# Kernel tuning notes

Measured on AMD Instinct MI355X. Metric: run time of the kernel, lower is better.

The kernel has to match this reference:

```python
import jax, jax.numpy as jnp
import numpy as np

N_NODES = 100000
N_EDGES = 3200000
F_IN = 1433
HID = 16
N_CLS = 7


def setup_inputs() -> dict:
    key = jax.random.key(0)
    k1, k2, k3, k4 = jax.random.split(key, 4)
    x = jax.random.normal(k1, (N_NODES, F_IN), dtype=jnp.float32)
    edge_index = jax.random.randint(k2, (2, N_EDGES), 0, N_NODES, dtype=jnp.int32)
    # Glorot-style init like GCNConv
    W1 = jax.random.normal(k3, (F_IN, HID), dtype=jnp.float32) * (1.0 / np.sqrt(F_IN))
    b1 = jnp.zeros((HID,), dtype=jnp.float32)
    W2 = jax.random.normal(k4, (HID, N_CLS), dtype=jnp.float32) * (1.0 / np.sqrt(HID))
    b2 = jnp.zeros((N_CLS,), dtype=jnp.float32)
    return {"x": x, "edge_index": edge_index, "W1": W1, "b1": b1, "W2": W2, "b2": b2}


def _gcn_conv(h, src, dst, W, b):
    # GCNConv with normalize=False: dense transform, then unweighted sum-aggregate
    # over incoming edges plus a self-loop (add_self_loops=True default), then bias.
    t = h @ W                                   # [N, out]
    agg = jax.ops.segment_sum(t[src], dst, num_segments=N_NODES)  # scatter-add over edges
    return agg + t + b                          # '+ t' = self-loop contribution


def reference(x, edge_index, W1, b1, W2, b2):
    src, dst = edge_index[0], edge_index[1]
    h = jax.nn.relu(_gcn_conv(x, src, dst, W1, b1))
    # F.dropout(training=False) is identity in eval mode
    out = _gcn_conv(h, src, dst, W2, b2)
    return out
```

## Files before the change

kernel.cpp:

```cpp
#include <hip/hip_runtime.h>

#define N_NODES 100000
#define N_EDGES 3200000
#define F_IN    1433
#define HID     16
#define N_CLS   7
#define NWINT   48
#define GB1     (N_NODES / 16)
#define QBLK    (N_EDGES / 4 / 256)
#define NTOT    ((long)N_NODES * F_IN)
#define NBKT    1024
#define NPBK    98
#define BCAP2   512
#define SRCM    0x1FFFF

typedef __attribute__((ext_vector_type(8))) short short8v;
typedef __attribute__((ext_vector_type(4))) float float4v;

typedef const __attribute__((address_space(1))) unsigned* gptr_t;
typedef __attribute__((address_space(3))) unsigned* lptr_t;

__device__ __forceinline__ unsigned short f2bf(float f) {
    unsigned u = __float_as_uint(f);
    u += 0x7fffu + ((u >> 16) & 1u);
    return (unsigned short)(u >> 16);
}

__device__ __forceinline__ void gll16(const float* g, float* lds) {
    gptr_t gp = (gptr_t)(unsigned long long)(uintptr_t)g;
    lptr_t lp = (lptr_t)(unsigned)(uintptr_t)lds;
    __builtin_amdgcn_global_load_lds(gp, lp, 16, 0, 0);
}

__global__ void prep_w1_kernel(const float* __restrict__ W1, short* __restrict__ w1f) {
    int w = blockIdx.x;
    int l = threadIdx.x;
    int col = l & 15;
    int kb = w * 32 + (l >> 4) * 8;
    short8v f;
#pragma unroll
    for (int i = 0; i < 8; ++i) {
        int k = kb + i;
        float v = (k < F_IN) ? W1[k * HID + col] : 0.f;
        f[i] = (short)f2bf(v);
    }
    *(short8v*)(w1f + ((size_t)w * 64 + l) * 8) = f;
}

__device__ __noinline__ void gemm_arm(int gid, const float* __restrict__ x,
                                      const short* __restrict__ w1f,
                                      float* __restrict__ t1) {
    __shared__ float xs[3][16][128];
    const int tid = threadIdx.x;
    const int s = tid >> 6;
    const int l = tid & 63;
    const int R0 = gid * 16;
    const int g = l >> 4;
    const int c = l & 15;

    short8v bf[12];
#pragma unroll
    for (int ph = 0; ph < 12; ++ph)
        bf[ph] = *(const short8v*)(w1f + ((size_t)((ph * 4 + s) * 64 + l)) * 8);

    const int row_a = 2 * s + (l >> 5);
    const int cs = l & 31;
    const bool last = (gid == GB1 - 1);

#define ISSUE(ph_)                                                              \
    {                                                                           \
        _Pragma("unroll")                                                       \
        for (int i = 0; i < 2; ++i) {                                           \
            int row = i * 8 + row_a;                                            \
            int gch = cs ^ (row & 7);                                           \
            long gi = (long)(R0 + row) * F_IN + (ph_) * 128 + gch * 4;          \
            if (last && gi > NTOT - 4) gi = NTOT - 4;                           \
            gll16(x + gi, &xs[(ph_) % 3][i * 8 + 2 * s][0]);                    \
        }                                                                       \
    }

    ISSUE(0); ISSUE(1);

    const int p0 = ((s * 8 + 2 * g) ^ (c & 7)) * 4;
    const int p1 = ((s * 8 + 2 * g + 1) ^ (c & 7)) * 4;

    float4v acc = {0.f, 0.f, 0.f, 0.f};
#pragma unroll
    for (int ph = 0; ph < 12; ++ph) {
        if (ph < 11) asm volatile("s_waitcnt vmcnt(2)" ::: "memory");
        else         asm volatile("s_waitcnt vmcnt(0)" ::: "memory");
        __builtin_amdgcn_sched_barrier(0);
        __builtin_amdgcn_s_barrier();
        if (ph + 2 < 12) ISSUE(ph + 2);
        const float* rowp = &xs[ph % 3][c][0];
        float4 lo = *(const float4*)(rowp + p0);
        float4 hi = *(const float4*)(rowp + p1);
        short8v af;
        af[0] = (short)f2bf(lo.x); af[1] = (short)f2bf(lo.y);
        af[2] = (short)f2bf(lo.z); af[3] = (short)f2bf(lo.w);
        af[4] = (short)f2bf(hi.x); af[5] = (short)f2bf(hi.y);
        af[6] = (short)f2bf(hi.z); af[7] = (short)f2bf(hi.w);
        acc = __builtin_amdgcn_mfma_f32_16x16x32_bf16(af, bf[ph], acc, 0, 0, 0);
    }
#undef ISSUE

    float* reds = &xs[0][0][0] + s * 256;
#pragma unroll
    for (int j = 0; j < 4; ++j) reds[l * 4 + j] = acc[j];
    __syncthreads();
    {
        int r = tid >> 4, cc = tid & 15;
        int idx = ((r >> 2) * 16 + cc) * 4 + (r & 3);
        float* rb = &xs[0][0][0];
        float vv = rb[idx] + rb[256 + idx] + rb[512 + idx] + rb[768 + idx];
        t1[(long)(R0 + r) * HID + cc] = vv;
    }
}

__device__ __noinline__ void fill_arm(int fbid, const int* __restrict__ src,
                                      const int* __restrict__ dst,
                                      int* __restrict__ cnt, int* __restrict__ bkt) {
    const int p = blockIdx.x & 7;
    int i = fbid * 256 + threadIdx.x;
    int4 s4 = ((const int4*)src)[i];
    int4 d4 = ((const int4*)dst)[i];
    unsigned b, dl; int pos;
    b = (unsigned)d4.x / NPBK; dl = (unsigned)d4.x - b * NPBK;
    pos = atomicAdd(&cnt[(p << 10) + b], 1);
    if (pos < BCAP2) bkt[((size_t)((p << 10) + b) << 9) + pos] = (int)((dl << 17) | (unsigned)s4.x);
    b = (unsigned)d4.y / NPBK; dl = (unsigned)d4.y - b * NPBK;
    pos = atomicAdd(&cnt[(p << 10) + b], 1);
    if (pos < BCAP2) bkt[((size_t)((p << 10) + b) << 9) + pos] = (int)((dl << 17) | (unsigned)s4.y);
    b = (unsigned)d4.z / NPBK; dl = (unsigned)d4.z - b * NPBK;
    pos = atomicAdd(&cnt[(p << 10) + b], 1);
    if (pos < BCAP2) bkt[((size_t)((p << 10) + b) << 9) + pos] = (int)((dl << 17) | (unsigned)s4.z);
    b = (unsigned)d4.w / NPBK; dl = (unsigned)d4.w - b * NPBK;
    pos = atomicAdd(&cnt[(p << 10) + b], 1);
    if (pos < BCAP2) bkt[((size_t)((p << 10) + b) << 9) + pos] = (int)((dl << 17) | (unsigned)s4.w);
}

__global__ __launch_bounds__(256) void fat1_kernel(const float* __restrict__ x,
                                                   const short* __restrict__ w1f,
                                                   float* __restrict__ t1,
                                                   const int* __restrict__ src,
                                                   const int* __restrict__ dst,
                                                   int* __restrict__ cnt,
                                                   int* __restrict__ bkt) {
    const int bid = blockIdx.x;
    if (bid % 3 == 2) fill_arm((bid - 2) / 3, src, dst, cnt, bkt);
    else              gemm_arm(bid - (bid + 1) / 3, x, w1f, t1);
}

__global__ __launch_bounds__(256) void agg1f_kernel(const float* __restrict__ t1,
                                                    const int* __restrict__ cnt,
                                                    const int* __restrict__ bkt,
                                                    const float* __restrict__ b1,
                                                    const float* __restrict__ W2,
                                                    float* __restrict__ t2p) {
    __shared__ int els[4096];
    __shared__ int ecsr[4096];
    __shared__ int dcnt[128], doff[128], dcur[128];
    __shared__ int pbase[9];
    __shared__ float hl[NPBK][16];
    const int b = blockIdx.x;
    const int t = threadIdx.x;
    if (t == 0) {
        int s = 0;
        for (int p = 0; p < 8; ++p) {
            pbase[p] = s;
            int ne = cnt[(p << 10) + b]; if (ne > BCAP2) ne = BCAP2;
            s += ne;
        }
        pbase[8] = s;
    }
    if (t < 128) dcnt[t] = 0;
    __syncthreads();
    const int nt = pbase[8];
    for (int p = 0; p < 8; ++p) {
        int base0 = pbase[p], ne = pbase[p + 1] - base0;
        const int* __restrict__ bp = bkt + ((size_t)((p << 10) + b) << 9);
        for (int e = t; e < ne; e += 256) els[base0 + e] = bp[e];
    }
    __syncthreads();
    for (int e = t; e < nt; e += 256) atomicAdd(&dcnt[els[e] >> 17], 1);
    __syncthreads();
    if (t < 128) doff[t] = dcnt[t];
    __syncthreads();
    for (int d = 1; d < 128; d <<= 1) {
        int add = (t < 128 && t >= d) ? doff[t - d] : 0;
        __syncthreads();
        if (t < 128) doff[t] += add;
        __syncthreads();
    }
    if (t < 128) dcur[t] = doff[t] - dcnt[t];
    __syncthreads();
    for (int e = t; e < nt; e += 256) {
        int v = els[e];
        int pos = atomicAdd(&dcur[v >> 17], 1);
        ecsr[pos] = v & SRCM;
    }
    __syncthreads();
    const int nbase = b * NPBK;
    {
        int q = t & 3;
        for (int nl = t >> 2; nl < NPBK; nl += 64) {
            int node = nbase + nl;
            if (node < N_NODES) {
                int o = doff[nl] - dcnt[nl];
                int d = dcnt[nl];
                float4 a0 = *(const float4*)(t1 + ((size_t)node * 16 + q * 4));
                float4 bb = *(const float4*)(b1 + q * 4);
                a0.x += bb.x; a0.y += bb.y; a0.z += bb.z; a0.w += bb.w;
                float4 a1 = {0.f, 0.f, 0.f, 0.f};
                int e = 0;
                for (; e + 4 <= d; e += 4) {
                    int s0 = ecsr[o + e],     s1 = ecsr[o + e + 1];
                    int s2 = ecsr[o + e + 2], s3 = ecsr[o + e + 3];
                    float4 v0 = *(const float4*)(t1 + ((size_t)s0 * 16 + q * 4));
                    float4 v1 = *(const float4*)(t1 + ((size_t)s1 * 16 + q * 4));
                    float4 v2 = *(const float4*)(t1 + ((size_t)s2 * 16 + q * 4));
                    float4 v3 = *(const float4*)(t1 + ((size_t)s3 * 16 + q * 4));
                    a0.x += v0.x; a0.y += v0.y; a0.z += v0.z; a0.w += v0.w;
                    a1.x += v1.x; a1.y += v1.y; a1.z += v1.z; a1.w += v1.w;
                    a0.x += v2.x; a0.y += v2.y; a0.z += v2.z; a0.w += v2.w;
                    a1.x += v3.x; a1.y += v3.y; a1.z += v3.z; a1.w += v3.w;
                }
                for (; e < d; ++e) {
                    int s = ecsr[o + e];
                    float4 v = *(const float4*)(t1 + ((size_t)s * 16 + q * 4));
                    a0.x += v.x; a0.y += v.y; a0.z += v.z; a0.w += v.w;
                }
                float4 r = {fmaxf(a0.x + a1.x, 0.f), fmaxf(a0.y + a1.y, 0.f),
                            fmaxf(a0.z + a1.z, 0.f), fmaxf(a0.w + a1.w, 0.f)};
                *(float4*)(&hl[nl][q * 4]) = r;
            }
        }
    }
    __syncthreads();
    for (int idx = t; idx < NPBK * 8; idx += 256) {
        int ln = idx >> 3, c = idx & 7;
        int node = nbase + ln;
        if (node < N_NODES) {
            float a = 0.f;
            if (c < N_CLS) {
#pragma unroll
                for (int j = 0; j < HID; ++j) a = fmaf(hl[ln][j], W2[j * N_CLS + c], a);
            }
            t2p[(size_t)node * 8 + c] = a;
        }
    }
}

__global__ __launch_bounds__(256) void agg2_kernel(const float* __restrict__ t2p,
                                                   const int* __restrict__ cnt,
                                                   const int* __restrict__ bkt,
                                                   const float* __restrict__ b2,
                                                   float* __restrict__ out) {
    __shared__ int els[4096];
    __shared__ int ecsr[4096];
    __shared__ int dcnt[128], doff[128], dcur[128];
    __shared__ int pbase[9];
    const int b = blockIdx.x;
    const int t = threadIdx.x;
    if (t == 0) {
        int s = 0;
        for (int p = 0; p < 8; ++p) {
            pbase[p] = s;
            int ne = cnt[(p << 10) + b]; if (ne > BCAP2) ne = BCAP2;
            s += ne;
        }
        pbase[8] = s;
    }
    if (t < 128) dcnt[t] = 0;
    __syncthreads();
    const int nt = pbase[8];
    for (int p = 0; p < 8; ++p) {
        int base0 = pbase[p], ne = pbase[p + 1] - base0;
        const int* __restrict__ bp = bkt + ((size_t)((p << 10) + b) << 9);
        for (int e = t; e < ne; e += 256) els[base0 + e] = bp[e];
    }
    __syncthreads();
    for (int e = t; e < nt; e += 256) atomicAdd(&dcnt[els[e] >> 17], 1);
    __syncthreads();
    if (t < 128) doff[t] = dcnt[t];
    __syncthreads();
    for (int d = 1; d < 128; d <<= 1) {
        int add = (t < 128 && t >= d) ? doff[t - d] : 0;
        __syncthreads();
        if (t < 128) doff[t] += add;
        __syncthreads();
    }
    if (t < 128) dcur[t] = doff[t] - dcnt[t];
    __syncthreads();
    for (int e = t; e < nt; e += 256) {
        int v = els[e];
        int pos = atomicAdd(&dcur[v >> 17], 1);
        ecsr[pos] = v & SRCM;
    }
    __syncthreads();
    const int nbase = b * NPBK;
    {
        int q = t & 1;
        for (int nl = t >> 1; nl < NPBK; nl += 128) {
            int node = nbase + nl;
            if (node < N_NODES) {
                int o = doff[nl] - dcnt[nl];
                int d = dcnt[nl];
                float4 a0 = *(const float4*)(t2p + ((size_t)node * 8 + q * 4));
                if (q == 0) {
                    a0.x += b2[0]; a0.y += b2[1]; a0.z += b2[2]; a0.w += b2[3];
                } else {
                    a0.x += b2[4]; a0.y += b2[5]; a0.z += b2[6];
                }
                float4 a1 = {0.f, 0.f, 0.f, 0.f};
                int e = 0;
                for (; e + 4 <= d; e += 4) {
                    int s0 = ecsr[o + e],     s1 = ecsr[o + e + 1];
                    int s2 = ecsr[o + e + 2], s3 = ecsr[o + e + 3];
                    float4 v0 = *(const float4*)(t2p + ((size_t)s0 * 8 + q * 4));
                    float4 v1 = *(const float4*)(t2p + ((size_t)s1 * 8 + q * 4));
                    float4 v2 = *(const float4*)(t2p + ((size_t)s2 * 8 + q * 4));
                    float4 v3 = *(const float4*)(t2p + ((size_t)s3 * 8 + q * 4));
                    a0.x += v0.x; a0.y += v0.y; a0.z += v0.z; a0.w += v0.w;
                    a1.x += v1.x; a1.y += v1.y; a1.z += v1.z; a1.w += v1.w;
                    a0.x += v2.x; a0.y += v2.y; a0.z += v2.z; a0.w += v2.w;
                    a1.x += v3.x; a1.y += v3.y; a1.z += v3.z; a1.w += v3.w;
                }
                for (; e < d; ++e) {
                    int s = ecsr[o + e];
                    float4 v = *(const float4*)(t2p + ((size_t)s * 8 + q * 4));
                    a0.x += v.x; a0.y += v.y; a0.z += v.z; a0.w += v.w;
                }
                float* op = out + (size_t)node * 7 + q * 4;
                op[0] = a0.x + a1.x; op[1] = a0.y + a1.y; op[2] = a0.z + a1.z;
                if (q == 0) op[3] = a0.w + a1.w;
            }
        }
    }
}


extern "C" void kernel_launch(void* const* d_in, const int* in_sizes, int n_in,
                              void* d_out, int out_size, void* d_ws, size_t ws_size,
                              hipStream_t stream) {
    const float* x  = (const float*)d_in[0];
    const int*   ei = (const int*)d_in[1];
    const float* W1 = (const float*)d_in[2];
    const float* b1 = (const float*)d_in[3];
    const float* W2 = (const float*)d_in[4];
    const float* b2 = (const float*)d_in[5];
    const int* src = ei;
    const int* dst = ei + N_EDGES;
    float* out = (float*)d_out;

    char* w = (char*)d_ws;
    float* t1  = (float*)w;  w += (size_t)N_NODES * HID * sizeof(float);
    float* t2p = (float*)w;  w += (size_t)N_NODES * 8 * sizeof(float);
    short* w1f = (short*)w;  w += (size_t)NWINT * 64 * 8 * sizeof(short);
    int* cnt   = (int*)w;    w += (size_t)8 * NBKT * sizeof(int);
    int* bkt   = (int*)w;    w += (size_t)8 * NBKT * BCAP2 * sizeof(int);

    (void)hipMemsetAsync(cnt, 0, (size_t)8 * NBKT * sizeof(int), stream);
    prep_w1_kernel<<<NWINT, 64, 0, stream>>>(W1, w1f);

    fat1_kernel<<<GB1 + QBLK, 256, 0, stream>>>(x, w1f, t1, src, dst, cnt, bkt);

    agg1f_kernel<<<NBKT, 256, 0, stream>>>(t1, cnt, bkt, b1, W2, t2p);
    agg2_kernel<<<NBKT, 256, 0, stream>>>(t2p, cnt, bkt, b2, out);
}
```

Before: 281.8 us.

## Load whole 8-row x tiles contiguously into LDS for GEMM arm

The GEMM arm now processes 8 rows per block and loads each row's full 1433-float span contiguously into a padded LDS buffer in one burst, instead of streaming 16-row by 128-column phases through a triple buffer. Each wave covers a contiguous K range of 384, and half of the MFMA lanes feed zeros because only 8 rows are valid. The fill/gemm block interleave changes from 1:2 to 1:4 to match the doubled GEMM block count. This aims at more contiguous global reads and less per-phase barrier overhead, but it wastes half the MFMA work, uses about 48KB of LDS per block (which lowers occupancy), and gives up the load/compute overlap.

```diff
diff --git a/kernel.cpp b/kernel.cpp
--- a/kernel.cpp
+++ b/kernel.cpp
@@ -6,9 +6,10 @@
 #define HID     16
 #define N_CLS   7
 #define NWINT   48
-#define GB1     (N_NODES / 16)
+#define GB1     (N_NODES / 8)
 #define QBLK    (N_EDGES / 4 / 256)
 #define NTOT    ((long)N_NODES * F_IN)
+#define LSTR    1444
 #define NBKT    1024
 #define NPBK    98
 #define BCAP2   512
@@ -50,69 +51,69 @@
 __device__ __noinline__ void gemm_arm(int gid, const float* __restrict__ x,
                                       const short* __restrict__ w1f,
                                       float* __restrict__ t1) {
-    __shared__ float xs[3][16][128];
+    __shared__ float xs[12288];
     const int tid = threadIdx.x;
     const int s = tid >> 6;
     const int l = tid & 63;
-    const int R0 = gid * 16;
+    const int R0 = gid * 8;
     const int g = l >> 4;
     const int c = l & 15;
 
     short8v bf[12];
 #pragma unroll
-    for (int ph = 0; ph < 12; ++ph)
-        bf[ph] = *(const short8v*)(w1f + ((size_t)((ph * 4 + s) * 64 + l)) * 8);
-
-    const int row_a = 2 * s + (l >> 5);
-    const int cs = l & 31;
-    const bool last = (gid == GB1 - 1);
-
-#define ISSUE(ph_)                                                              \
-    {                                                                           \
-        _Pragma("unroll")                                                       \
-        for (int i = 0; i < 2; ++i) {                                           \
-            int row = i * 8 + row_a;                                            \
-            int gch = cs ^ (row & 7);                                           \
-            long gi = (long)(R0 + row) * F_IN + (ph_) * 128 + gch * 4;          \
-            if (last && gi > NTOT - 4) gi = NTOT - 4;                           \
-            gll16(x + gi, &xs[(ph_) % 3][i * 8 + 2 * s][0]);                    \
-        }                                                                       \
-    }
-
-    ISSUE(0); ISSUE(1);
-
-    const int p0 = ((s * 8 + 2 * g) ^ (c & 7)) * 4;
-    const int p1 = ((s * 8 + 2 * g + 1) ^ (c & 7)) * 4;
-
+    for (int wl = 0; wl < 12; ++wl)
+        bf[wl] = *(const short8v*)(w1f + ((size_t)((s * 12 + wl) * 64 + l)) * 8);
+
+    if (gid != GB1 - 1) {
+#pragma unroll
+        for (int j = 0; j < 12; ++j) {
+            int df = j * 1024 + tid * 4;
+            unsigned row = (unsigned)df / (unsigned)LSTR;
+            unsigned col = (unsigned)df - row * (unsigned)LSTR;
+            long src = (row < 8 && col < 1433)
+                           ? (long)(R0 + (int)row) * F_IN + col
+                           : 0;
+            gll16(x + src, &xs[df]);
+        }
+        __syncthreads();
+    } else {
+        for (int idx = tid; idx < 8 * LSTR; idx += 256) {
+            int row = idx / LSTR, col = idx - row * LSTR;
+            float v = (col < F_IN) ? x[(long)(R0 + row) * F_IN + col] : 0.f;
+            xs[idx] = v;
+        }
+        for (int idx = 8 * LSTR + tid; idx < 12288; idx += 256) xs[idx] = 0.f;
+        __syncthreads();
+    }
+
+    const int kb = s * 384;
+    const bool act = (c < 8);
     float4v acc = {0.f, 0.f, 0.f, 0.f};
 #pragma unroll
-    for (int ph = 0; ph < 12; ++ph) {
-        if (ph < 11) asm volatile("s_waitcnt vmcnt(2)" ::: "memory");
-        else         asm volatile("s_waitcnt vmcnt(0)" ::: "memory");
-        __builtin_amdgcn_sched_barrier(0);
-        __builtin_amdgcn_s_barrier();
-        if (ph + 2 < 12) ISSUE(ph + 2);
-        const float* rowp = &xs[ph % 3][c][0];
-        float4 lo = *(const float4*)(rowp + p0);
-        float4 hi = *(const float4*)(rowp + p1);
+    for (int wl = 0; wl < 12; ++wl) {
+        int off = c * LSTR + kb + wl * 32 + g * 8;
+        float4 lo = {0.f, 0.f, 0.f, 0.f}, hi = {0.f, 0.f, 0.f, 0.f};
+        if (act) {
+            lo = *(const float4*)(&xs[off]);
+            hi = *(const float4*)(&xs[off + 4]);
+        }
         short8v af;
         af[0] = (short)f2bf(lo.x); af[1] = (short)f2bf(lo.y);
         af[2] = (short)f2bf(lo.z); af[3] = (short)f2bf(lo.w);
         af[4] = (short)f2bf(hi.x); af[5] = (short)f2bf(hi.y);
         af[6] = (short)f2bf(hi.z); af[7] = (short)f2bf(hi.w);
-        acc = __builtin_amdgcn_mfma_f32_16x16x32_bf16(af, bf[ph], acc, 0, 0, 0);
-    }
-#undef ISSUE
-
-    float* reds = &xs[0][0][0] + s * 256;
+        acc = __builtin_amdgcn_mfma_f32_16x16x32_bf16(af, bf[wl], acc, 0, 0, 0);
+    }
+
+    __syncthreads();
+    float* reds = &xs[s * 256];
 #pragma unroll
     for (int j = 0; j < 4; ++j) reds[l * 4 + j] = acc[j];
     __syncthreads();
-    {
+    if (tid < 128) {
         int r = tid >> 4, cc = tid & 15;
         int idx = ((r >> 2) * 16 + cc) * 4 + (r & 3);
-        float* rb = &xs[0][0][0];
-        float vv = rb[idx] + rb[256 + idx] + rb[512 + idx] + rb[768 + idx];
+        float vv = xs[idx] + xs[256 + idx] + xs[512 + idx] + xs[768 + idx];
         t1[(long)(R0 + r) * HID + cc] = vv;
     }
 }
@@ -147,8 +148,8 @@
                                                    int* __restrict__ cnt,
                                                    int* __restrict__ bkt) {
     const int bid = blockIdx.x;
-    if (bid % 3 == 2) fill_arm((bid - 2) / 3, src, dst, cnt, bkt);
-    else              gemm_arm(bid - (bid + 1) / 3, x, w1f, t1);
+    if (bid % 5 == 4) fill_arm((bid - 4) / 5, src, dst, cnt, bkt);
+    else              gemm_arm(bid - (bid + 1) / 5, x, w1f, t1);
 }
 
 __global__ __launch_bounds__(256) void agg1f_kernel(const float* __restrict__ t1,
```

Result: faster. 270.8 us (median of 2 runs) (-3.9%).
